# Performance work log

Hardware: AMD Instinct MI355X
Metric: run time of the kernel (lower is better)

## Reference

```python
import jax, jax.numpy as jnp
import numpy as np

V, T_BLOCK, D, H, L, HS = 32000, 1024, 1024, 16, 6, 64
B, T = 4, 1024
EPS = 1e-5


def setup_inputs() -> dict:
    key = jax.random.key(0)
    ks = jax.random.split(key, 12)
    s = 0.02  # init std, matches _init_weights
    return {
        'input_tokens': jax.random.randint(ks[0], (B, T), 0, V),
        'tok_emb': jax.random.normal(ks[1], (V, D), jnp.float32) * s,
        'pos_emb': jax.random.normal(ks[2], (T_BLOCK, D), jnp.float32) * s,
        'Wq': jax.random.normal(ks[3], (L, H, D, HS), jnp.float32) * s,
        'Wk': jax.random.normal(ks[4], (L, H, D, HS), jnp.float32) * s,
        'Wv': jax.random.normal(ks[5], (L, H, D, HS), jnp.float32) * s,
        'Wo': jax.random.normal(ks[6], (L, D, D), jnp.float32) * s,
        'bo': jnp.zeros((L, D), jnp.float32),
        'ln1_g': jnp.ones((L, D), jnp.float32),
        'ln1_b': jnp.zeros((L, D), jnp.float32),
        'ln2_g': jnp.ones((L, D), jnp.float32),
        'ln2_b': jnp.zeros((L, D), jnp.float32),
        'W1': jax.random.normal(ks[7], (L, D, 4 * D), jnp.float32) * s,
        'b1': jnp.zeros((L, 4 * D), jnp.float32),
        'W2': jax.random.normal(ks[8], (L, 4 * D, D), jnp.float32) * s,
        'b2': jnp.zeros((L, D), jnp.float32),
        'lnf_g': jnp.ones((D,), jnp.float32),
        'lnf_b': jnp.zeros((D,), jnp.float32),
        'W_out': jax.random.normal(ks[9], (D, V), jnp.float32) * s,
        'b_out': jnp.zeros((V,), jnp.float32),
    }


def _layer_norm(x, g, b):
    mu = jnp.mean(x, axis=-1, keepdims=True)
    var = jnp.mean(jnp.square(x - mu), axis=-1, keepdims=True)
    return (x - mu) * jax.lax.rsqrt(var + EPS) * g + b


def _attn(x, Wq, Wk, Wv, Wo, bo, causal_mask):
    # x: [B,T,D]; Wq/Wk/Wv: [H,D,hs] (per-head linears, bias=False)
    q = jnp.einsum('btd,hds->bhts', x, Wq)
    k = jnp.einsum('btd,hds->bhts', x, Wk)
    v = jnp.einsum('btd,hds->bhts', x, Wv)
    scores = jnp.einsum('bhts,bhus->bhtu', q, k) * (HS ** -0.5)
    scores = jnp.where(causal_mask, scores, -jnp.inf)
    w = jax.nn.softmax(scores, axis=-1)  # dropout=0.0 -> identity
    o = jnp.einsum('bhtu,bhus->bhts', w, v)
    # concat heads in order, then projection
    o = o.transpose(0, 2, 1, 3).reshape(x.shape[0], x.shape[1], H * HS)
    return o @ Wo + bo


def reference(input_tokens, tok_emb, pos_emb, Wq, Wk, Wv, Wo, bo,
              ln1_g, ln1_b, ln2_g, ln2_b, W1, b1, W2, b2,
              lnf_g, lnf_b, W_out, b_out):
    Bc, Tc = input_tokens.shape
    x = tok_emb[input_tokens] + pos_emb[:Tc]  # [B,T,D]
    mask = jnp.tril(jnp.ones((Tc, Tc), bool))[None, None]  # [1,1,T,T]
    for l in range(L):
        x = x + _attn(_layer_norm(x, ln1_g[l], ln1_b[l]),
                      Wq[l], Wk[l], Wv[l], Wo[l], bo[l], mask)
        h = _layer_norm(x, ln2_g[l], ln2_b[l])
        x = x + jax.nn.relu(h @ W1[l] + b1[l]) @ W2[l] + b2[l]
    x = _layer_norm(x, lnf_g, lnf_b)
    logits = x @ W_out + b_out  # [B,T,V]
    return logits
```

## Files before the change

### kernel.cpp

```cpp
#include <hip/hip_runtime.h>
#include <hip/hip_bf16.h>

#define HS 64
#define NH 16
#define DMODEL 1024
#define SEQ 1024
#define NB 4
#define NL 6
#define VOCAB 32000
#define EPS_LN 1e-5f

static constexpr int ROWS = NB * SEQ;

typedef float f32x4 __attribute__((ext_vector_type(4)));
typedef short bf16x8 __attribute__((ext_vector_type(8)));
typedef unsigned short u16x8 __attribute__((ext_vector_type(8)));
typedef unsigned short u16x4 __attribute__((ext_vector_type(4)));

__device__ __forceinline__ unsigned short f2b(float f) {
  __hip_bfloat16 h = __float2bfloat16(f);
  return *reinterpret_cast<unsigned short*>(&h);
}
__device__ __forceinline__ void gload_lds16(const void* g, void* l) {
  __builtin_amdgcn_global_load_lds(
      (const __attribute__((address_space(1))) void*)g,
      (__attribute__((address_space(3))) void*)l, 16, 0, 0);
}
#define MFMA16 __builtin_amdgcn_mfma_f32_16x16x32_bf16
#define EXP2F __builtin_amdgcn_exp2f

__global__ __launch_bounds__(256) void embed_kernel(
    const int* __restrict__ tokens, const float* __restrict__ tok_emb,
    const float* __restrict__ pos_emb, float* __restrict__ x) {
  int row = blockIdx.x;
  int t = row & (SEQ - 1);
  int tok = tokens[row];
  int d = threadIdx.x * 4;
  float4 te = *(const float4*)(tok_emb + (size_t)tok * DMODEL + d);
  float4 pe = *(const float4*)(pos_emb + (size_t)t * DMODEL + d);
  te.x += pe.x; te.y += pe.y; te.z += pe.z; te.w += pe.w;
  *(float4*)(x + (size_t)row * DMODEL + d) = te;
}

__global__ __launch_bounds__(256) void ln_kernel(
    const float* __restrict__ in, unsigned short* __restrict__ outp,
    const float* __restrict__ g, const float* __restrict__ b) {
  int row = blockIdx.x;
  int tid = threadIdx.x;
  const float* xr = in + (size_t)row * DMODEL;
  float4 v4 = *(const float4*)(xr + tid * 4);
  float s = v4.x + v4.y + v4.z + v4.w;
  float s2 = v4.x * v4.x + v4.y * v4.y + v4.z * v4.z + v4.w * v4.w;
#pragma unroll
  for (int off = 32; off > 0; off >>= 1) {
    s  += __shfl_down(s, off, 64);
    s2 += __shfl_down(s2, off, 64);
  }
  __shared__ float red[8];
  __shared__ float stats[2];
  int wv = tid >> 6, lane = tid & 63;
  if (lane == 0) { red[wv] = s; red[4 + wv] = s2; }
  __syncthreads();
  if (tid == 0) {
    float ts = red[0] + red[1] + red[2] + red[3];
    float ts2 = red[4] + red[5] + red[6] + red[7];
    float mu = ts * (1.0f / DMODEL);
    float var = ts2 * (1.0f / DMODEL) - mu * mu;
    stats[0] = mu;
    stats[1] = rsqrtf(var + EPS_LN);
  }
  __syncthreads();
  float mu = stats[0], rstd = stats[1];
  float4 g4 = *(const float4*)(g + tid * 4);
  float4 b4 = *(const float4*)(b + tid * 4);
  u16x4 o;
  o[0] = f2b((v4.x - mu) * rstd * g4.x + b4.x);
  o[1] = f2b((v4.y - mu) * rstd * g4.y + b4.y);
  o[2] = f2b((v4.z - mu) * rstd * g4.z + b4.z);
  o[3] = f2b((v4.w - mu) * rstd * g4.w + b4.w);
  *(u16x4*)(outp + (size_t)row * DMODEL + tid * 4) = o;
}

__global__ __launch_bounds__(256) void transconv(
    const float* __restrict__ in, unsigned short* __restrict__ outp, int K, int N) {
  __shared__ float tile[64][33];
  size_t zoff = (size_t)blockIdx.z * K * N;
  in += zoff;
  outp += zoff;
  int n0 = blockIdx.x * 32, k0 = blockIdx.y * 64;
  int tx = threadIdx.x & 31, ty = threadIdx.x >> 5;
#pragma unroll
  for (int i = 0; i < 8; ++i)
    tile[ty + i * 8][tx] = in[(size_t)(k0 + ty + i * 8) * N + n0 + tx];
  __syncthreads();
  int n = threadIdx.x >> 3;
  int kq = (threadIdx.x & 7) * 8;
  u16x8 o8;
#pragma unroll
  for (int j = 0; j < 8; ++j) o8[j] = f2b(tile[kq + j][n]);
  *(u16x8*)(outp + (size_t)(n0 + n) * K + k0 + kq) = o8;
}

__global__ __launch_bounds__(256) void qkv_transconv(
    const float* __restrict__ Wq, const float* __restrict__ Wk,
    const float* __restrict__ Wv, unsigned short* __restrict__ outp) {
  __shared__ float tile[64][33];
  int z = blockIdx.z;
  int l = z / 48;
  int r = z % 48;
  int which = r >> 4, h = r & 15;
  const float* W = (which == 0 ? Wq : which == 1 ? Wk : Wv) +
                   ((size_t)l * NH + h) * DMODEL * HS;
  int s0 = blockIdx.x * 32, d0 = blockIdx.y * 64;
  int tx = threadIdx.x & 31, ty = threadIdx.x >> 5;
#pragma unroll
  for (int i = 0; i < 8; ++i)
    tile[ty + i * 8][tx] = W[(size_t)(d0 + ty + i * 8) * HS + s0 + tx];
  __syncthreads();
  unsigned short* ob = outp + ((size_t)l * 3072 + which * 1024 + h * 64) * DMODEL;
  int n = threadIdx.x >> 3;
  int kq = (threadIdx.x & 7) * 8;
  u16x8 o8;
#pragma unroll
  for (int j = 0; j < 8; ++j) o8[j] = f2b(tile[kq + j][n]);
  *(u16x8*)(ob + (size_t)(s0 + n) * DMODEL + d0 + kq) = o8;
}

#define EPI_LOGITS 0
#define EPI_RES 1
#define EPI_RELU 2
#define EPI_QKV 3

template <int EPI, int BM_, bool N_INNER>
__global__ __launch_bounds__(512, 2) void mmX(
    const unsigned short* __restrict__ A, const unsigned short* __restrict__ Bt,
    const float* __restrict__ bias, const float* __restrict__ res,
    float* __restrict__ outf, unsigned short* __restrict__ ob0,
    unsigned short* __restrict__ ob1, unsigned short* __restrict__ ob2,
    int M, int N, int K) {
  constexpr int NA = BM_ / 64;
  constexpr int AP = BM_ / 128;
  constexpr int MFRAG = BM_ / 32;
  __shared__ __align__(16) unsigned short LDS[2][(BM_ + 256) * 64];
  const int tid = threadIdx.x;
  const int lane = tid & 63, w = tid >> 6;
  const int wm2 = w >> 2, wn4 = w & 3;
  const int l15 = lane & 15, l4 = lane >> 4;

  const int nM = M / BM_, nN = N >> 8;
  const int nwg = nM * nN;
  int bid = blockIdx.x;
  int wg = (bid & 7) * (nwg >> 3) + (bid >> 3);
  int mb, nb;
  if (N_INNER) { nb = wg % nN; mb = wg / nN; }
  else         { mb = wg % nM; nb = wg / nM; }
  const int m0 = mb * BM_, n0 = nb * 256;

  const int srow = tid >> 3;
  const int scolb = (tid & 7) * 16;
  const int swst = (srow & 7) << 4;
  const char* aS = (const char*)A + ((size_t)(m0 + srow) * K) * 2 + (scolb ^ swst);
  const char* bS = (const char*)Bt + ((size_t)(n0 + srow) * K) * 2 + (scolb ^ swst);
  const size_t rstep = (size_t)64 * K * 2;

  const int kb0 = l4 * 16;
  const int swz = (l15 & 7) << 4;

  const int NT = K >> 6;
  f32x4 acc[MFRAG][4] = {};
  bf16x8 bv[4][2], avA[AP][2], avB[AP][2];

#define STAGEX(tt)                                                          \
  {                                                                         \
    unsigned short* ad = &LDS[(tt) & 1][0] + (size_t)tid * 8;               \
    unsigned short* bd = &LDS[(tt) & 1][BM_ * 64] + (size_t)tid * 8;        \
    size_t ko = (size_t)(tt) * 128;                                         \
    _Pragma("unroll")                                                       \
    for (int j = 0; j < NA; ++j) gload_lds16(aS + ko + j * rstep, ad + j * 4096); \
    _Pragma("unroll")                                                       \
    for (int j = 0; j < 4; ++j) gload_lds16(bS + ko + j * rstep, bd + j * 4096);  \
  }

#define READA(dst, p)                                                       \
  _Pragma("unroll")                                                         \
  for (int mm = 0; mm < AP; ++mm)                                           \
  _Pragma("unroll")                                                         \
    for (int ks = 0; ks < 2; ++ks)                                          \
      dst[mm][ks] = *(const bf16x8*)(ab + (AP * (p) + mm) * 2048 +          \
                                     ((kb0 + 64 * ks) ^ swz));

#define GROUP(src, p)                                                       \
  __builtin_amdgcn_s_setprio(1);                                            \
  _Pragma("unroll")                                                         \
  for (int ks = 0; ks < 2; ++ks)                                            \
  _Pragma("unroll")                                                         \
    for (int mm = 0; mm < AP; ++mm)                                         \
    _Pragma("unroll")                                                       \
      for (int ni = 0; ni < 4; ++ni)                                        \
        acc[AP * (p) + mm][ni] =                                            \
            MFMA16(src[mm][ks], bv[ni][ks], acc[AP * (p) + mm][ni], 0, 0, 0);\
  __builtin_amdgcn_s_setprio(0);

  STAGEX(0)
  STAGEX(1)

  for (int t = 0; t < NT; ++t) {
    if (t < NT - 1) {
      if constexpr (BM_ == 256) asm volatile("s_waitcnt vmcnt(8)" ::: "memory");
      else                      asm volatile("s_waitcnt vmcnt(6)" ::: "memory");
    } else {
      asm volatile("s_waitcnt vmcnt(0)" ::: "memory");
    }
    __builtin_amdgcn_s_barrier();
    __builtin_amdgcn_sched_barrier(0);
    const char* ab = (const char*)&LDS[t & 1][0] +
                     (size_t)(wm2 * (BM_ / 2) + l15) * 128;
    const char* bb = (const char*)&LDS[t & 1][BM_ * 64] +
                     (size_t)(wn4 * 64 + l15) * 128;
#pragma unroll
    for (int ni = 0; ni < 4; ++ni)
#pragma unroll
      for (int ks = 0; ks < 2; ++ks)
        bv[ni][ks] = *(const bf16x8*)(bb + ni * 2048 + ((kb0 + 64 * ks) ^ swz));
    READA(avA, 0)
    READA(avB, 1)
    GROUP(avA, 0)
    READA(avA, 2)
    GROUP(avB, 1)
    READA(avB, 3)
    GROUP(avA, 2)
    asm volatile("s_waitcnt lgkmcnt(0)" ::: "memory");
    __builtin_amdgcn_sched_barrier(0);
    __builtin_amdgcn_s_barrier();
    __builtin_amdgcn_sched_barrier(0);
    if (t + 2 < NT) STAGEX(t + 2)
    GROUP(avB, 3)
  }
#undef STAGEX
#undef READA
#undef GROUP

  int rbase = m0 + wm2 * (BM_ / 2) + (l4 << 2);
  int cbase = n0 + wn4 * 64 + l15;

  if constexpr (EPI == EPI_LOGITS) {
    float* fl = (float*)&LDS[0][0];
#pragma unroll
    for (int half = 0; half < 2; ++half) {
      __syncthreads();
      if (wm2 == half) {
#pragma unroll
        for (int ni = 0; ni < 4; ++ni) {
          float bvv = bias[cbase + ni * 16];
          int cl = wn4 * 64 + l15 + ni * 16;
#pragma unroll
          for (int mi = 0; mi < MFRAG; ++mi) {
#pragma unroll
            for (int r = 0; r < 4; ++r) {
              int rl = mi * 16 + (l4 << 2) + r;
              fl[rl * 256 + (cl ^ (((rl >> 2) & 7) << 2))] = acc[mi][ni][r] + bvv;
            }
          }
        }
      }
      __syncthreads();
#pragma unroll
      for (int j = 0; j < 16; ++j) {
        int idx = j * 512 + tid;
        int rl = idx >> 6;
        int cc = (idx & 63) << 2;
        f32x4 v4 = *(const f32x4*)&fl[rl * 256 + (cc ^ (((rl >> 2) & 7) << 2))];
        float* gp = outf + (size_t)(m0 + half * 128 + rl) * N + n0 + cc;
        __builtin_nontemporal_store(v4, (f32x4*)gp);
      }
    }
  } else {
#pragma unroll
    for (int ni = 0; ni < 4; ++ni) {
      int col = cbase + ni * 16;
      float bvv = 0.f;
      if (EPI != EPI_QKV) bvv = bias[col];
      if (EPI == EPI_QKV) {
        int which = col >> 10;
        int c2 = col & 1023;
        int h = c2 >> 6, s = c2 & 63;
#pragma unroll
        for (int mi = 0; mi < MFRAG; ++mi) {
          f32x4 a4 = acc[mi][ni];
          int row0 = rbase + mi * 16;
          int bb2 = row0 >> 10, t0 = row0 & 1023;
          if (which == 2) {
            u16x4 pk;
            pk[0] = f2b(a4[0]); pk[1] = f2b(a4[1]); pk[2] = f2b(a4[2]); pk[3] = f2b(a4[3]);
            *(u16x4*)(ob2 + ((((size_t)bb2 * NH + h) * HS) + s) * SEQ + t0) = pk;
          } else {
            unsigned short* dst = (which == 0) ? ob0 : ob1;
#pragma unroll
            for (int r = 0; r < 4; ++r)
              dst[((((size_t)bb2 * NH) + h) * SEQ + t0 + r) * HS + s] = f2b(a4[r]);
          }
        }
      } else {
#pragma unroll
        for (int mi = 0; mi < MFRAG; ++mi) {
          f32x4 a4 = acc[mi][ni];
#pragma unroll
          for (int r = 0; r < 4; ++r) {
            int rowg = rbase + mi * 16 + r;
            size_t off = (size_t)rowg * N + col;
            float v = a4[r] + bvv;
            if (EPI == EPI_RES) outf[off] = v + res[off];
            else if (EPI == EPI_RELU) ob0[off] = f2b(fmaxf(v, 0.f));
          }
        }
      }
    }
  }
}

template <int EPI>
__global__ __launch_bounds__(256, 2) void mmP(
    const unsigned short* __restrict__ A, const unsigned short* __restrict__ Bt,
    const float* __restrict__ bias, const float* __restrict__ res,
    float* __restrict__ outf, unsigned short* __restrict__ ob0,
    int M, int N, int K) {
  __shared__ __align__(16) unsigned short LDS[2][16384];
  const int tid = threadIdx.x;
  const int lane = tid & 63, w = tid >> 6;
  const int wm2 = w >> 1, wn2 = w & 1;
  const int l15 = lane & 15, l4 = lane >> 4;

  const int nM = M >> 7, nN = N >> 7;
  const int nwg = nM * nN;
  int bid = blockIdx.x;
  int wg = (bid & 7) * (nwg >> 3) + (bid >> 3);
  int mb = wg % nM, nb = wg / nM;
  const int m0 = mb * 128, n0 = nb * 128;

  const int srow = tid >> 3;
  const int scolb = (tid & 7) * 16;
  const int swst = (srow & 7) << 4;
  const char* aS = (const char*)A + ((size_t)(m0 + srow) * K) * 2 + (scolb ^ swst);
  const char* bS = (const char*)Bt + ((size_t)(n0 + srow) * K) * 2 + (scolb ^ swst);
  const size_t rstep = (size_t)32 * K * 2;

  const int kb0 = l4 * 16;
  const int swz = (l15 & 7) << 4;

  const int NT = K >> 6;
  f32x4 acc[4][4] = {};
  bf16x8 bv[4][2];

#define STAGEX(tt)                                                          \
  {                                                                         \
    unsigned short* ad = &LDS[(tt) & 1][0] + (size_t)tid * 8;               \
    unsigned short* bd = &LDS[(tt) & 1][8192] + (size_t)tid * 8;            \
    size_t ko = (size_t)(tt) * 128;                                         \
    _Pragma("unroll")                                                       \
    for (int j = 0; j < 4; ++j) gload_lds16(aS + ko + j * rstep, ad + j * 2048); \
    _Pragma("unroll")                                                       \
    for (int j = 0; j < 4; ++j) gload_lds16(bS + ko + j * rstep, bd + j * 2048); \
  }

#define RDA(dst, mi)                                                        \
  dst##k0 = *(const bf16x8*)(ab + (mi) * 2048 + (kb0 ^ swz));               \
  dst##k1 = *(const bf16x8*)(ab + (mi) * 2048 + ((kb0 + 64) ^ swz));

#define GROUP(src, mi)                                                      \
  __builtin_amdgcn_s_setprio(1);                                            \
  _Pragma("unroll")                                                         \
  for (int ni = 0; ni < 4; ++ni)                                            \
    acc[mi][ni] = MFMA16(src##k0, bv[ni][0], acc[mi][ni], 0, 0, 0);         \
  _Pragma("unroll")                                                         \
  for (int ni = 0; ni < 4; ++ni)                                            \
    acc[mi][ni] = MFMA16(src##k1, bv[ni][1], acc[mi][ni], 0, 0, 0);         \
  __builtin_amdgcn_s_setprio(0);

  STAGEX(0)
  STAGEX(1)

  for (int t = 0; t < NT; ++t) {
    if (t < NT - 1) asm volatile("s_waitcnt vmcnt(8)" ::: "memory");
    else            asm volatile("s_waitcnt vmcnt(0)" ::: "memory");
    __builtin_amdgcn_s_barrier();
    __builtin_amdgcn_sched_barrier(0);
    const char* ab = (const char*)&LDS[t & 1][0] + (size_t)(wm2 * 64 + l15) * 128;
    const char* bb = (const char*)&LDS[t & 1][8192] + (size_t)(wn2 * 64 + l15) * 128;
    bf16x8 aEk0, aEk1, aOk0, aOk1;
#pragma unroll
    for (int ni = 0; ni < 4; ++ni) {
      bv[ni][0] = *(const bf16x8*)(bb + ni * 2048 + (kb0 ^ swz));
      bv[ni][1] = *(const bf16x8*)(bb + ni * 2048 + ((kb0 + 64) ^ swz));
    }
    RDA(aE, 0)
    GROUP(aE, 0)
    RDA(aO, 1)
    GROUP(aO, 1)
    RDA(aE, 2)
    GROUP(aE, 2)
    RDA(aO, 3)
    asm volatile("s_waitcnt lgkmcnt(0)" ::: "memory");
    __builtin_amdgcn_sched_barrier(0);
    __builtin_amdgcn_s_barrier();
    __builtin_amdgcn_sched_barrier(0);
    if (t + 2 < NT) STAGEX(t + 2)
    GROUP(aO, 3)
  }
#undef STAGEX
#undef RDA
#undef GROUP

  int rbase = m0 + wm2 * 64 + (l4 << 2);
  int cbase = n0 + wn2 * 64 + l15;
#pragma unroll
  for (int ni = 0; ni < 4; ++ni) {
    int col = cbase + ni * 16;
    float bvv = bias[col];
#pragma unroll
    for (int mi = 0; mi < 4; ++mi) {
      f32x4 a4 = acc[mi][ni];
#pragma unroll
      for (int r = 0; r < 4; ++r) {
        int rowg = rbase + mi * 16 + r;
        size_t off = (size_t)rowg * N + col;
        float v = a4[r] + bvv;
        if (EPI == EPI_RES) outf[off] = v + res[off];
        else if (EPI == EPI_RELU) ob0[off] = f2b(fmaxf(v, 0.f));
      }
    }
  }
}

__global__ __launch_bounds__(512) void attn_mfma(
    const unsigned short* __restrict__ q, const unsigned short* __restrict__ k,
    const unsigned short* __restrict__ vt, unsigned short* __restrict__ outp) {
  __shared__ __align__(16) unsigned short S[32768];
  unsigned short* Ks = S;
  unsigned short* Vs = S + 16384;
  int qt = blockIdx.x, bh = blockIdx.y;
  int tid = threadIdx.x;
  int lane = tid & 63, w = tid >> 6;
  int l15 = lane & 15, l4 = lane >> 4;

  const unsigned short* qb = q + (size_t)bh * SEQ * HS;
  const unsigned short* kb = k + (size_t)bh * SEQ * HS;
  const unsigned short* vb = vt + (size_t)bh * HS * SEQ;

  int q_l = w * 16 + l15;
  int q_g = qt * 128 + q_l;
  bf16x8 qf[2];
  qf[0] = *(const bf16x8*)(qb + (size_t)q_g * HS + l4 * 8);
  qf[1] = *(const bf16x8*)(qb + (size_t)q_g * HS + l4 * 8 + 32);

  int kOff[2], vOff[2];
#pragma unroll
  for (int j = 0; j < 2; ++j) {
    int idx = tid + j * 512;
    kOff[j] = (idx >> 7) * 16 * HS + (idx & 15) * HS + ((idx >> 4) & 7) * 8;
    vOff[j] = ((idx >> 8) * 16 + (idx & 15)) * SEQ + ((idx >> 4) & 15) * 8;
  }

#define ASTAGE(tt)                                                           \
  {                                                                          \
    int bsel = ((tt) & 1) * 8192;                                            \
    const unsigned short* ksrc = kb + (size_t)(tt) * 128 * HS;               \
    const unsigned short* vsrc = vb + (tt) * 128;                            \
    _Pragma("unroll")                                                        \
    for (int j = 0; j < 2; ++j)                                              \
      gload_lds16(ksrc + kOff[j], Ks + bsel + (size_t)(tid + j * 512) * 8);  \
    _Pragma("unroll")                                                        \
    for (int j = 0; j < 2; ++j)                                              \
      gload_lds16(vsrc + vOff[j], Vs + bsel + (size_t)(tid + j * 512) * 8);  \
  }

  f32x4 o[4] = {};
  float mrun = -3e38f, lrun = 0.f;
  int baseLane = 32 * (l4 & 1) + l15;
  bool hi_t = (l4 >> 1) != 0;
  const float CSC = 0.125f * 1.44269504f;
  const float THR = 8.0f / CSC;

  int nt2 = qt + 1;
  ASTAGE(0)

  for (int kt = 0; kt < nt2; ++kt) {
    asm volatile("s_waitcnt vmcnt(0)" ::: "memory");
    __builtin_amdgcn_s_barrier();
    __builtin_amdgcn_sched_barrier(0);
    if (kt + 1 < nt2) ASTAGE(kt + 1)
    const unsigned short* Kb = Ks + (kt & 1) * 8192;
    const unsigned short* Vb = Vs + (kt & 1) * 8192;

    f32x4 s[8];
    __builtin_amdgcn_s_setprio(1);
#pragma unroll
    for (int t = 0; t < 8; ++t) {
      bf16x8 kf0 = *(const bf16x8*)(Kb + ((size_t)(t * 8 + l4) * 16 + l15) * 8);
      bf16x8 kf1 = *(const bf16x8*)(Kb + ((size_t)(t * 8 + l4 + 4) * 16 + l15) * 8);
      s[t] = (f32x4){0.f, 0.f, 0.f, 0.f};
      s[t] = MFMA16(kf0, qf[0], s[t], 0, 0, 0);
      s[t] = MFMA16(kf1, qf[1], s[t], 0, 0, 0);
    }
    __builtin_amdgcn_s_setprio(0);

    if (kt == nt2 - 1) {
      int keybase = kt * 128 + 4 * l4;
#pragma unroll
      for (int t = 0; t < 8; ++t)
#pragma unroll
        for (int r = 0; r < 4; ++r)
          if (keybase + 16 * t + r > q_g) s[t][r] = -3e38f;
    }
    float mx = -3e38f;
#pragma unroll
    for (int t = 0; t < 8; ++t)
#pragma unroll
      for (int r = 0; r < 4; ++r) mx = fmaxf(mx, s[t][r]);
    mx = fmaxf(mx, __shfl_xor(mx, 16, 64));
    mx = fmaxf(mx, __shfl_xor(mx, 32, 64));
    if (!__all(mx - mrun <= THR)) {
      float mnew = fmaxf(mrun, mx);
      float sc = EXP2F((mrun - mnew) * CSC);
      lrun *= sc;
#pragma unroll
      for (int t2 = 0; t2 < 4; ++t2)
#pragma unroll
        for (int r = 0; r < 4; ++r) o[t2][r] *= sc;
      mrun = mnew;
    }
    float mc = mrun * CSC;
    float ps = 0.f;
#pragma unroll
    for (int t = 0; t < 8; ++t)
#pragma unroll
      for (int r = 0; r < 4; ++r) {
        float e = EXP2F(__builtin_fmaf(s[t][r], CSC, -mc));
        s[t][r] = e;
        ps += e;
      }
    ps += __shfl_xor(ps, 16, 64);
    ps += __shfl_xor(ps, 32, 64);
    lrun += ps;

    int pd[8][2];
#pragma unroll
    for (int t = 0; t < 8; ++t)
#pragma unroll
      for (int h = 0; h < 2; ++h)
        pd[t][h] = (int)f2b(s[t][2 * h]) | ((int)f2b(s[t][2 * h + 1]) << 16);

#pragma unroll
    for (int kk = 0; kk < 4; ++kk) {
      int a0 = __shfl(pd[2 * kk][0], baseLane, 64);
      int b0 = __shfl(pd[2 * kk + 1][0], baseLane, 64);
      int a1 = __shfl(pd[2 * kk][1], baseLane, 64);
      int b1 = __shfl(pd[2 * kk + 1][1], baseLane, 64);
      int a2 = __shfl(pd[2 * kk][0], baseLane + 16, 64);
      int b2 = __shfl(pd[2 * kk + 1][0], baseLane + 16, 64);
      int a3 = __shfl(pd[2 * kk][1], baseLane + 16, 64);
      int b3 = __shfl(pd[2 * kk + 1][1], baseLane + 16, 64);
      union { int4 i4; bf16x8 v; } yu;
      yu.i4.x = hi_t ? b0 : a0;
      yu.i4.y = hi_t ? b1 : a1;
      yu.i4.z = hi_t ? b2 : a2;
      yu.i4.w = hi_t ? b3 : a3;
      __builtin_amdgcn_s_setprio(1);
#pragma unroll
      for (int t2 = 0; t2 < 4; ++t2) {
        bf16x8 vf = *(const bf16x8*)(Vb + ((size_t)(t2 * 16 + kk * 4 + l4) * 16 + l15) * 8);
        o[t2] = MFMA16(vf, yu.v, o[t2], 0, 0, 0);
      }
      __builtin_amdgcn_s_setprio(0);
    }
  }
#undef ASTAGE

  __syncthreads();
  float inv = 1.0f / lrun;
  unsigned short* Ol = S;
#pragma unroll
  for (int t2 = 0; t2 < 4; ++t2) {
    u16x4 p4;
#pragma unroll
    for (int r = 0; r < 4; ++r) p4[r] = f2b(o[t2][r] * inv);
    *(u16x4*)(Ol + (size_t)q_l * 72 + 16 * t2 + 4 * l4) = p4;
  }
  __syncthreads();
  int row = tid >> 2, hs0 = (tid & 3) * 16;
  int bidx = bh >> 4, h = bh & 15;
  size_t gbase = ((size_t)bidx * SEQ + qt * 128 + row) * DMODEL + h * HS + hs0;
  u16x8 r0 = *(const u16x8*)(Ol + (size_t)row * 72 + hs0);
  u16x8 r1 = *(const u16x8*)(Ol + (size_t)row * 72 + hs0 + 8);
  *(u16x8*)(outp + gbase) = r0;
  *(u16x8*)(outp + gbase + 8) = r1;
}

extern "C" void kernel_launch(void* const* d_in, const int* in_sizes, int n_in,
                              void* d_out, int out_size, void* d_ws, size_t ws_size,
                              hipStream_t stream) {
  const int*   tokens  = (const int*)d_in[0];
  const float* tok_emb = (const float*)d_in[1];
  const float* pos_emb = (const float*)d_in[2];
  const float* Wq      = (const float*)d_in[3];
  const float* Wk      = (const float*)d_in[4];
  const float* Wv      = (const float*)d_in[5];
  const float* Wo      = (const float*)d_in[6];
  const float* bo      = (const float*)d_in[7];
  const float* ln1_g   = (const float*)d_in[8];
  const float* ln1_b   = (const float*)d_in[9];
  const float* ln2_g   = (const float*)d_in[10];
  const float* ln2_b   = (const float*)d_in[11];
  const float* W1      = (const float*)d_in[12];
  const float* b1      = (const float*)d_in[13];
  const float* W2      = (const float*)d_in[14];
  const float* b2      = (const float*)d_in[15];
  const float* lnf_g   = (const float*)d_in[16];
  const float* lnf_b   = (const float*)d_in[17];
  const float* W_out   = (const float*)d_in[18];
  const float* b_out   = (const float*)d_in[19];
  float* logits = (float*)d_out;

  char* p = (char*)d_ws;
  float* x = (float*)p;            p += (size_t)ROWS * DMODEL * 4;
  unsigned short* hb = (unsigned short*)p;  p += (size_t)ROWS * DMODEL * 2;
  unsigned short* qb = (unsigned short*)p;  p += (size_t)ROWS * DMODEL * 2;
  unsigned short* kb = (unsigned short*)p;  p += (size_t)ROWS * DMODEL * 2;
  unsigned short* vtb = (unsigned short*)p; p += (size_t)ROWS * DMODEL * 2;
  unsigned short* att = (unsigned short*)p; p += (size_t)ROWS * DMODEL * 2;
  unsigned short* hid = (unsigned short*)p; p += (size_t)ROWS * 4 * DMODEL * 2;
  unsigned short* qkvt = (unsigned short*)p; p += (size_t)NL * 3 * DMODEL * DMODEL * 2;
  unsigned short* wot = (unsigned short*)p;  p += (size_t)NL * DMODEL * DMODEL * 2;
  unsigned short* w1t = (unsigned short*)p;  p += (size_t)NL * 4 * DMODEL * DMODEL * 2;
  unsigned short* w2t = (unsigned short*)p;  p += (size_t)NL * 4 * DMODEL * DMODEL * 2;
  unsigned short* woutt = (unsigned short*)p; p += (size_t)VOCAB * DMODEL * 2;

  transconv<<<dim3(32, 16, NL), 256, 0, stream>>>(Wo, wot, DMODEL, DMODEL);
  transconv<<<dim3(128, 16, NL), 256, 0, stream>>>(W1, w1t, DMODEL, 4 * DMODEL);
  transconv<<<dim3(32, 64, NL), 256, 0, stream>>>(W2, w2t, 4 * DMODEL, DMODEL);
  transconv<<<dim3(1000, 16, 1), 256, 0, stream>>>(W_out, woutt, DMODEL, VOCAB);
  qkv_transconv<<<dim3(2, 16, NL * 48), 256, 0, stream>>>(Wq, Wk, Wv, qkvt);

  embed_kernel<<<ROWS, 256, 0, stream>>>(tokens, tok_emb, pos_emb, x);

  for (int l = 0; l < NL; ++l) {
    ln_kernel<<<ROWS, 256, 0, stream>>>(x, hb, ln1_g + l * DMODEL, ln1_b + l * DMODEL);
    mmX<EPI_QKV, 128, false><<<384, 512, 0, stream>>>(
        hb, qkvt + (size_t)l * 3 * DMODEL * DMODEL, nullptr, nullptr,
        nullptr, qb, kb, vtb, ROWS, 3 * DMODEL, DMODEL);
    attn_mfma<<<dim3(SEQ / 128, NB * NH), 512, 0, stream>>>(qb, kb, vtb, att);
    mmP<EPI_RES><<<256, 256, 0, stream>>>(
        att, wot + (size_t)l * DMODEL * DMODEL, bo + l * DMODEL, x,
        x, nullptr, ROWS, DMODEL, DMODEL);
    ln_kernel<<<ROWS, 256, 0, stream>>>(x, hb, ln2_g + l * DMODEL, ln2_b + l * DMODEL);
    mmP<EPI_RELU><<<1024, 256, 0, stream>>>(
        hb, w1t + (size_t)l * 4 * DMODEL * DMODEL, b1 + (size_t)l * 4 * DMODEL, nullptr,
        nullptr, hid, ROWS, 4 * DMODEL, DMODEL);
    mmP<EPI_RES><<<256, 256, 0, stream>>>(
        hid, w2t + (size_t)l * 4 * DMODEL * DMODEL, b2 + l * DMODEL, x,
        x, nullptr, ROWS, DMODEL, 4 * DMODEL);
  }

  ln_kernel<<<ROWS, 256, 0, stream>>>(x, hb, lnf_g, lnf_b);
  mmX<EPI_LOGITS, 256, true><<<2000, 512, 0, stream>>>(
      hb, woutt, b_out, nullptr, logits, nullptr, nullptr, nullptr,
      ROWS, VOCAB, DMODEL);
}
```

Baseline: 1.735 ms.

## Make logits GEMM persistent over M tiles and move QKV to mmP

The logits GEMM becomes a persistent kernel. It launches 250 workgroups, and each one loops over 8 M-tiles for a fixed 256-column N block, so the same W_out slice is re-streamed while it stays hot in cache. Separately, the QKV projection moves from the 128-row mmX variant to the smaller-tile mmP kernel, whose epilogue gains the QKV scatter path. The persistent loop costs parallelism: 250 workgroups is about one wave on the device, with no tail overlap.

```diff
diff --git a/kernel.cpp b/kernel.cpp
--- a/kernel.cpp
+++ b/kernel.cpp
@@ -131,44 +131,37 @@
 #define EPI_RELU 2
 #define EPI_QKV 3
 
-template <int EPI, int BM_, bool N_INNER>
-__global__ __launch_bounds__(512, 2) void mmX(
+template <int MSPAN>
+__global__ __launch_bounds__(512, 2) void mmL(
     const unsigned short* __restrict__ A, const unsigned short* __restrict__ Bt,
-    const float* __restrict__ bias, const float* __restrict__ res,
-    float* __restrict__ outf, unsigned short* __restrict__ ob0,
-    unsigned short* __restrict__ ob1, unsigned short* __restrict__ ob2,
+    const float* __restrict__ bias, float* __restrict__ outf,
     int M, int N, int K) {
-  constexpr int NA = BM_ / 64;
-  constexpr int AP = BM_ / 128;
-  constexpr int MFRAG = BM_ / 32;
+  constexpr int BM_ = 256;
+  constexpr int NA = 4;
+  constexpr int AP = 2;
+  constexpr int MFRAG = 8;
   __shared__ __align__(16) unsigned short LDS[2][(BM_ + 256) * 64];
   const int tid = threadIdx.x;
   const int lane = tid & 63, w = tid >> 6;
   const int wm2 = w >> 2, wn4 = w & 3;
   const int l15 = lane & 15, l4 = lane >> 4;
 
-  const int nM = M / BM_, nN = N >> 8;
-  const int nwg = nM * nN;
+  const int nN = N >> 8;
   int bid = blockIdx.x;
-  int wg = (bid & 7) * (nwg >> 3) + (bid >> 3);
-  int mb, nb;
-  if (N_INNER) { nb = wg % nN; mb = wg / nN; }
-  else         { mb = wg % nM; nb = wg / nM; }
-  const int m0 = mb * BM_, n0 = nb * 256;
+  const int nb = bid >> 1;
+  const int mb0 = (bid & 1) * MSPAN;
+  const int n0 = nb * 256;
 
   const int srow = tid >> 3;
   const int scolb = (tid & 7) * 16;
   const int swst = (srow & 7) << 4;
-  const char* aS = (const char*)A + ((size_t)(m0 + srow) * K) * 2 + (scolb ^ swst);
   const char* bS = (const char*)Bt + ((size_t)(n0 + srow) * K) * 2 + (scolb ^ swst);
   const size_t rstep = (size_t)64 * K * 2;
 
   const int kb0 = l4 * 16;
   const int swz = (l15 & 7) << 4;
-
   const int NT = K >> 6;
-  f32x4 acc[MFRAG][4] = {};
-  bf16x8 bv[4][2], avA[AP][2], avB[AP][2];
+  (void)nN;
 
 #define STAGEX(tt)                                                          \
   {                                                                         \
@@ -201,49 +194,45 @@
             MFMA16(src[mm][ks], bv[ni][ks], acc[AP * (p) + mm][ni], 0, 0, 0);\
   __builtin_amdgcn_s_setprio(0);
 
-  STAGEX(0)
-  STAGEX(1)
-
-  for (int t = 0; t < NT; ++t) {
-    if (t < NT - 1) {
-      if constexpr (BM_ == 256) asm volatile("s_waitcnt vmcnt(8)" ::: "memory");
-      else                      asm volatile("s_waitcnt vmcnt(6)" ::: "memory");
-    } else {
-      asm volatile("s_waitcnt vmcnt(0)" ::: "memory");
-    }
-    __builtin_amdgcn_s_barrier();
-    __builtin_amdgcn_sched_barrier(0);
-    const char* ab = (const char*)&LDS[t & 1][0] +
-                     (size_t)(wm2 * (BM_ / 2) + l15) * 128;
-    const char* bb = (const char*)&LDS[t & 1][BM_ * 64] +
-                     (size_t)(wn4 * 64 + l15) * 128;
-#pragma unroll
-    for (int ni = 0; ni < 4; ++ni)
-#pragma unroll
-      for (int ks = 0; ks < 2; ++ks)
-        bv[ni][ks] = *(const bf16x8*)(bb + ni * 2048 + ((kb0 + 64 * ks) ^ swz));
-    READA(avA, 0)
-    READA(avB, 1)
-    GROUP(avA, 0)
-    READA(avA, 2)
-    GROUP(avB, 1)
-    READA(avB, 3)
-    GROUP(avA, 2)
-    asm volatile("s_waitcnt lgkmcnt(0)" ::: "memory");
-    __builtin_amdgcn_sched_barrier(0);
-    __builtin_amdgcn_s_barrier();
-    __builtin_amdgcn_sched_barrier(0);
-    if (t + 2 < NT) STAGEX(t + 2)
-    GROUP(avB, 3)
-  }
-#undef STAGEX
-#undef READA
-#undef GROUP
-
-  int rbase = m0 + wm2 * (BM_ / 2) + (l4 << 2);
-  int cbase = n0 + wn4 * 64 + l15;
-
-  if constexpr (EPI == EPI_LOGITS) {
+  for (int mo = 0; mo < MSPAN; ++mo) {
+    const int m0 = (mb0 + mo) * BM_;
+    const char* aS = (const char*)A + ((size_t)(m0 + srow) * K) * 2 + (scolb ^ swst);
+    f32x4 acc[MFRAG][4] = {};
+    bf16x8 bv[4][2], avA[AP][2], avB[AP][2];
+
+    STAGEX(0)
+    STAGEX(1)
+
+    for (int t = 0; t < NT; ++t) {
+      if (t < NT - 1) asm volatile("s_waitcnt vmcnt(8)" ::: "memory");
+      else            asm volatile("s_waitcnt vmcnt(0)" ::: "memory");
+      __builtin_amdgcn_s_barrier();
+      __builtin_amdgcn_sched_barrier(0);
+      const char* ab = (const char*)&LDS[t & 1][0] +
+                       (size_t)(wm2 * (BM_ / 2) + l15) * 128;
+      const char* bb = (const char*)&LDS[t & 1][BM_ * 64] +
+                       (size_t)(wn4 * 64 + l15) * 128;
+#pragma unroll
+      for (int ni = 0; ni < 4; ++ni)
+#pragma unroll
+        for (int ks = 0; ks < 2; ++ks)
+          bv[ni][ks] = *(const bf16x8*)(bb + ni * 2048 + ((kb0 + 64 * ks) ^ swz));
+      READA(avA, 0)
+      READA(avB, 1)
+      GROUP(avA, 0)
+      READA(avA, 2)
+      GROUP(avB, 1)
+      READA(avB, 3)
+      GROUP(avA, 2)
+      asm volatile("s_waitcnt lgkmcnt(0)" ::: "memory");
+      __builtin_amdgcn_sched_barrier(0);
+      __builtin_amdgcn_s_barrier();
+      __builtin_amdgcn_sched_barrier(0);
+      if (t + 2 < NT) STAGEX(t + 2)
+      GROUP(avB, 3)
+    }
+
+    int cbase = n0 + wn4 * 64 + l15;
     float* fl = (float*)&LDS[0][0];
 #pragma unroll
     for (int half = 0; half < 2; ++half) {
@@ -274,48 +263,11 @@
         __builtin_nontemporal_store(v4, (f32x4*)gp);
       }
     }
-  } else {
-#pragma unroll
-    for (int ni = 0; ni < 4; ++ni) {
-      int col = cbase + ni * 16;
-      float bvv = 0.f;
-      if (EPI != EPI_QKV) bvv = bias[col];
-      if (EPI == EPI_QKV) {
-        int which = col >> 10;
-        int c2 = col & 1023;
-        int h = c2 >> 6, s = c2 & 63;
-#pragma unroll
-        for (int mi = 0; mi < MFRAG; ++mi) {
-          f32x4 a4 = acc[mi][ni];
-          int row0 = rbase + mi * 16;
-          int bb2 = row0 >> 10, t0 = row0 & 1023;
-          if (which == 2) {
-            u16x4 pk;
-            pk[0] = f2b(a4[0]); pk[1] = f2b(a4[1]); pk[2] = f2b(a4[2]); pk[3] = f2b(a4[3]);
-            *(u16x4*)(ob2 + ((((size_t)bb2 * NH + h) * HS) + s) * SEQ + t0) = pk;
-          } else {
-            unsigned short* dst = (which == 0) ? ob0 : ob1;
-#pragma unroll
-            for (int r = 0; r < 4; ++r)
-              dst[((((size_t)bb2 * NH) + h) * SEQ + t0 + r) * HS + s] = f2b(a4[r]);
-          }
-        }
-      } else {
-#pragma unroll
-        for (int mi = 0; mi < MFRAG; ++mi) {
-          f32x4 a4 = acc[mi][ni];
-#pragma unroll
-          for (int r = 0; r < 4; ++r) {
-            int rowg = rbase + mi * 16 + r;
-            size_t off = (size_t)rowg * N + col;
-            float v = a4[r] + bvv;
-            if (EPI == EPI_RES) outf[off] = v + res[off];
-            else if (EPI == EPI_RELU) ob0[off] = f2b(fmaxf(v, 0.f));
-          }
-        }
-      }
-    }
-  }
+    __syncthreads();
+  }
+#undef STAGEX
+#undef READA
+#undef GROUP
 }
 
 template <int EPI>
@@ -323,6 +275,7 @@
     const unsigned short* __restrict__ A, const unsigned short* __restrict__ Bt,
     const float* __restrict__ bias, const float* __restrict__ res,
     float* __restrict__ outf, unsigned short* __restrict__ ob0,
+    unsigned short* __restrict__ ob1, unsigned short* __restrict__ ob2,
     int M, int N, int K) {
   __shared__ __align__(16) unsigned short LDS[2][16384];
   const int tid = threadIdx.x;
@@ -415,17 +368,39 @@
 #pragma unroll
   for (int ni = 0; ni < 4; ++ni) {
     int col = cbase + ni * 16;
-    float bvv = bias[col];
-#pragma unroll
-    for (int mi = 0; mi < 4; ++mi) {
-      f32x4 a4 = acc[mi][ni];
-#pragma unroll
-      for (int r = 0; r < 4; ++r) {
-        int rowg = rbase + mi * 16 + r;
-        size_t off = (size_t)rowg * N + col;
-        float v = a4[r] + bvv;
-        if (EPI == EPI_RES) outf[off] = v + res[off];
-        else if (EPI == EPI_RELU) ob0[off] = f2b(fmaxf(v, 0.f));
+    if (EPI == EPI_QKV) {
+      int which = col >> 10;
+      int c2 = col & 1023;
+      int h = c2 >> 6, s = c2 & 63;
+#pragma unroll
+      for (int mi = 0; mi < 4; ++mi) {
+        f32x4 a4 = acc[mi][ni];
+        int row0 = rbase + mi * 16;
+        int bb2 = row0 >> 10, t0 = row0 & 1023;
+        if (which == 2) {
+          u16x4 pk;
+          pk[0] = f2b(a4[0]); pk[1] = f2b(a4[1]); pk[2] = f2b(a4[2]); pk[3] = f2b(a4[3]);
+          *(u16x4*)(ob2 + ((((size_t)bb2 * NH + h) * HS) + s) * SEQ + t0) = pk;
+        } else {
+          unsigned short* dst = (which == 0) ? ob0 : ob1;
+#pragma unroll
+          for (int r = 0; r < 4; ++r)
+            dst[((((size_t)bb2 * NH) + h) * SEQ + t0 + r) * HS + s] = f2b(a4[r]);
+        }
+      }
+    } else {
+      float bvv = bias[col];
+#pragma unroll
+      for (int mi = 0; mi < 4; ++mi) {
+        f32x4 a4 = acc[mi][ni];
+#pragma unroll
+        for (int r = 0; r < 4; ++r) {
+          int rowg = rbase + mi * 16 + r;
+          size_t off = (size_t)rowg * N + col;
+          float v = a4[r] + bvv;
+          if (EPI == EPI_RES) outf[off] = v + res[off];
+          else if (EPI == EPI_RELU) ob0[off] = f2b(fmaxf(v, 0.f));
+        }
       }
     }
   }
@@ -644,24 +619,22 @@
 
   for (int l = 0; l < NL; ++l) {
     ln_kernel<<<ROWS, 256, 0, stream>>>(x, hb, ln1_g + l * DMODEL, ln1_b + l * DMODEL);
-    mmX<EPI_QKV, 128, false><<<384, 512, 0, stream>>>(
+    mmP<EPI_QKV><<<768, 256, 0, stream>>>(
         hb, qkvt + (size_t)l * 3 * DMODEL * DMODEL, nullptr, nullptr,
         nullptr, qb, kb, vtb, ROWS, 3 * DMODEL, DMODEL);
     attn_mfma<<<dim3(SEQ / 128, NB * NH), 512, 0, stream>>>(qb, kb, vtb, att);
     mmP<EPI_RES><<<256, 256, 0, stream>>>(
         att, wot + (size_t)l * DMODEL * DMODEL, bo + l * DMODEL, x,
-        x, nullptr, ROWS, DMODEL, DMODEL);
+        x, nullptr, nullptr, nullptr, ROWS, DMODEL, DMODEL);
     ln_kernel<<<ROWS, 256, 0, stream>>>(x, hb, ln2_g + l * DMODEL, ln2_b + l * DMODEL);
     mmP<EPI_RELU><<<1024, 256, 0, stream>>>(
         hb, w1t + (size_t)l * 4 * DMODEL * DMODEL, b1 + (size_t)l * 4 * DMODEL, nullptr,
-        nullptr, hid, ROWS, 4 * DMODEL, DMODEL);
+        nullptr, hid, nullptr, nullptr, ROWS, 4 * DMODEL, DMODEL);
     mmP<EPI_RES><<<256, 256, 0, stream>>>(
         hid, w2t + (size_t)l * 4 * DMODEL * DMODEL, b2 + l * DMODEL, x,
-        x, nullptr, ROWS, DMODEL, 4 * DMODEL);
+        x, nullptr, nullptr, nullptr, ROWS, DMODEL, 4 * DMODEL);
   }
 
   ln_kernel<<<ROWS, 256, 0, stream>>>(x, hb, lnf_g, lnf_b);
-  mmX<EPI_LOGITS, 256, true><<<2000, 512, 0, stream>>>(
-      hb, woutt, b_out, nullptr, logits, nullptr, nullptr, nullptr,
-      ROWS, VOCAB, DMODEL);
-}
+  mmL<8><<<250, 512, 0, stream>>>(hb, woutt, b_out, logits, ROWS, VOCAB, DMODEL);
+}
```

Result: slower. 1.812 ms (+4.5%).
